# Optimization experiments

Hardware: AMD Instinct MI355X
Metric: run time of the kernel (lower is better)

Reference implementation:

```python
import jax, jax.numpy as jnp
import numpy as np

B, D, H, K = 2048, 1024, 64, 3
SKIP = 4  # first 4 dims only accumulate into ai, produce no heads


def setup_inputs() -> dict:
    key = jax.random.key(0)
    ks = jax.random.split(key, 6)
    return {
        "x": jax.random.normal(ks[0], (B, D), jnp.float32),
        "W": jax.random.normal(ks[1], (H, D), jnp.float32) * (2.0 / (H + 1)) ** 0.5,
        "c": jax.random.normal(ks[2], (1, H), jnp.float32) * 0.0,
        "Vmean": jax.random.normal(ks[3], (D, H, K), jnp.float32) * (2.0 / (H + K)) ** 0.5,
        "Valpha": jax.random.normal(ks[4], (D, H, K), jnp.float32) * (2.0 / (H + K)) ** 0.5,
        "Vstd": jax.random.normal(ks[5], (D, H, K), jnp.float32) * (2.0 / (H + K)) ** 0.5,
        "bmean": jnp.zeros((D, K), jnp.float32),
        "balpha": jnp.zeros((D, K), jnp.float32),
        "bstd": jnp.zeros((D, K), jnp.float32),
    }


def reference(x, W, c, Vmean, Valpha, Vstd, bmean, balpha, bstd):
    # ai before processing dim d is c + sum_{j<d} x[:, j] * W[:, j]^T.
    # This is a cumulative sum of per-dim rank-1 contributions -> one cumsum.
    contrib = x[:, :, None] * W.T[None, :, :]          # [B, D, H]
    prefix = c[None, :, :] + jnp.cumsum(contrib, axis=1)  # prefix[:, d] = c + sum_{j<=d}
    # h_i for dim d (d >= SKIP) uses ai = prefix[:, d-1]
    h = jax.nn.relu(prefix[:, SKIP - 1:-1, :])          # [B, D-SKIP, H]

    mean = jnp.einsum("bdh,dhk->bdk", h, Vmean[SKIP:]) + bmean[SKIP:]
    std = jax.nn.sigmoid(
        jnp.einsum("bdh,dhk->bdk", h, Vstd[SKIP:]) + bstd[SKIP:]
    ) * 2.0 + 0.6  # 10**-1 + 0.5
    alpha = jax.nn.softmax(
        jnp.einsum("bdh,dhk->bdk", h, Valpha[SKIP:]) + balpha[SKIP:], axis=-1
    )
    return (mean, std, alpha)  # each [B, D-4, K]
```

## Files before the change

### kernel.cpp

```cpp
#include <hip/hip_runtime.h>
#include <hip/hip_bf16.h>

#define B 2048
#define D 1024
#define H 64
#define DOUT (D - 4)
#define T 64
#define DC 16

typedef __attribute__((ext_vector_type(8))) short short8;
typedef __attribute__((ext_vector_type(4))) float f32x4;

#define WS_S  0
#define WS_VB (T * B * H / 2)

__device__ __forceinline__ unsigned short f2h_u(float f) {
    union { _Float16 h; unsigned short u; } v; v.h = (_Float16)f; return v.u;
}
__device__ __forceinline__ float h2f_u(unsigned short s) {
    union { unsigned short u; _Float16 h; } v; v.u = s; return (float)v.h;
}
__device__ __forceinline__ unsigned short f2bf(float f) {
    union { float f; unsigned int u; } v; v.f = f;
    unsigned int r = (v.u + 0x7FFFu + ((v.u >> 16) & 1u)) >> 16;
    return (unsigned short)r;
}
__device__ __forceinline__ unsigned cvtpk_bf16(float lo, float hi) {
    unsigned d;
    asm("v_cvt_pk_bf16_f32 %0, %1, %2" : "=v"(d) : "v"(lo), "v"(hi));
    return d;
}

union U8 { unsigned u[4]; short8 s; };

__global__ __launch_bounds__(256) void k_pack(const float* __restrict__ Vm,
                                              const float* __restrict__ Va,
                                              const float* __restrict__ Vs,
                                              uint4* __restrict__ VbP) {
    const int idx = blockIdx.x * 256 + threadIdx.x;
    const int l   = idx & 63;
    const int ks  = (idx >> 6) & 1;
    const int d   = idx >> 7;
    const int m   = l & 15;
    const int h0  = ks * 32 + (l >> 4) * 8;

    const float* src = nullptr;
    int k = 0;
    if (m < 3)                { src = Vm; k = m; }
    else if (m >= 4 && m < 7) { src = Vs; k = m - 4; }
    else if (m >= 8 && m < 11){ src = Va; k = m - 8; }

    unsigned u[4] = {0u, 0u, 0u, 0u};
    if (src) {
#pragma unroll
        for (int i = 0; i < 4; ++i) {
            unsigned short lo = f2bf(src[((size_t)d * H + h0 + 2 * i) * 3 + k]);
            unsigned short hi = f2bf(src[((size_t)d * H + h0 + 2 * i + 1) * 3 + k]);
            u[i] = ((unsigned)hi << 16) | lo;
        }
    }
    VbP[idx] = make_uint4(u[0], u[1], u[2], u[3]);
}

__global__ __launch_bounds__(512) void k_prefix(const float* __restrict__ x,
                                                const float* __restrict__ W,
                                                const float* __restrict__ cvec,
                                                unsigned short* __restrict__ S) {
    __shared__ float wt[64 * 68];
    __shared__ float xl[8 * 64];
    const int tid  = threadIdx.x;
    const int lane = tid & 63;
    const int w    = tid >> 6;
    const int b    = blockIdx.x * 8 + w;

    float run = cvec[lane];
    for (int c = 0; c < 16; ++c) {
        __syncthreads();
        {
            const int h = tid >> 3, dc = (tid & 7) * 8;
            const float* src = W + (size_t)h * D + c * 64 + dc;
            float4 v0 = *(const float4*)src;
            float4 v1 = *(const float4*)(src + 4);
            float* dst = wt + h * 68 + dc;
            *(float4*)dst = v0;
            *(float4*)(dst + 4) = v1;
        }
        xl[w * 64 + lane] = x[(size_t)b * D + c * 64 + lane];
        __syncthreads();
#pragma unroll
        for (int dg = 0; dg < 16; ++dg) {
            if ((dg & 3) == 1) {
                const int t = 4 * c + (dg >> 2);
                S[((size_t)t * B + b) * H + lane] = f2h_u(run);
            }
            float4 w4 = *(const float4*)(wt + lane * 68 + dg * 4);
            float4 x4 = *(const float4*)(xl + w * 64 + dg * 4);
            run = fmaf(x4.x, w4.x, run);
            run = fmaf(x4.y, w4.y, run);
            run = fmaf(x4.z, w4.z, run);
            run = fmaf(x4.w, w4.w, run);
        }
    }
}

__global__ __launch_bounds__(256, 2) void k_main(const float* __restrict__ x,
                                                 const float* __restrict__ W,
                                                 const unsigned short* __restrict__ S,
                                                 const uint4* __restrict__ VbP,
                                                 const float* __restrict__ bm,
                                                 const float* __restrict__ ba,
                                                 const float* __restrict__ bs,
                                                 float* __restrict__ out) {
    __shared__ short8 vbsh[DC][2][64];
    __shared__ float  wshf[DC][64];
    __shared__ float  xsf[DC][256];
    __shared__ float  bshf[DC][16];

    const int tid    = threadIdx.x;
    const int lane   = tid & 63;
    const int w      = tid >> 6;
    const int t      = blockIdx.y;
    const int bx     = blockIdx.x;
    const int dstart = 16 * t + 4;
    const int dvalid = D - dstart;
    const int r      = lane & 15;
    const int qq     = lane >> 4;

    {
        const uint4* vsrc = VbP + (size_t)dstart * 128;
        uint4* vdst = (uint4*)vbsh;
#pragma unroll
        for (int q = 0; q < 8; ++q) {
            const int j = q * 256 + tid;
            if (j < dvalid * 128) vdst[j] = vsrc[j];
        }
        {
            const int h = tid >> 2, part = tid & 3;
            if (dstart + part * 4 < D) {
                float4 v = *(const float4*)(W + (size_t)h * D + dstart + part * 4);
                wshf[part * 4 + 0][h] = v.x;
                wshf[part * 4 + 1][h] = v.y;
                wshf[part * 4 + 2][h] = v.z;
                wshf[part * 4 + 3][h] = v.w;
            }
        }
        {
            const float* xr = x + (size_t)(bx * 256 + tid) * D + dstart;
#pragma unroll
            for (int part = 0; part < 4; ++part) {
                if (dstart + part * 4 < D) {
                    float4 v = *(const float4*)(xr + part * 4);
                    xsf[part * 4 + 0][tid] = v.x;
                    xsf[part * 4 + 1][tid] = v.y;
                    xsf[part * 4 + 2][tid] = v.z;
                    xsf[part * 4 + 3][tid] = v.w;
                }
            }
        }
        {
            const int dl = tid >> 4, m = tid & 15;
            const int d = dstart + dl;
            float v = 0.f;
            if (d < D) {
                if (m < 3)                 v = bm[(size_t)d * 3 + m];
                else if (m >= 4 && m < 7)  v = bs[(size_t)d * 3 + m - 4];
                else if (m >= 8 && m < 11) v = ba[(size_t)d * 3 + m - 8];
            }
            bshf[dl][m] = v;
        }
    }

    float a_[4][2][8];
#pragma unroll
    for (int bt = 0; bt < 4; ++bt) {
#pragma unroll
        for (int ks = 0; ks < 2; ++ks) {
            const unsigned short* sp =
                S + ((size_t)t * B + bx * 256 + w * 64 + bt * 16 + r) * H + ks * 32 + qq * 8;
            uint4 u = *(const uint4*)sp;
            a_[bt][ks][0] = h2f_u((unsigned short)(u.x & 0xffff));
            a_[bt][ks][1] = h2f_u((unsigned short)(u.x >> 16));
            a_[bt][ks][2] = h2f_u((unsigned short)(u.y & 0xffff));
            a_[bt][ks][3] = h2f_u((unsigned short)(u.y >> 16));
            a_[bt][ks][4] = h2f_u((unsigned short)(u.z & 0xffff));
            a_[bt][ks][5] = h2f_u((unsigned short)(u.z >> 16));
            a_[bt][ks][6] = h2f_u((unsigned short)(u.w & 0xffff));
            a_[bt][ks][7] = h2f_u((unsigned short)(u.w >> 16));
        }
    }
    __syncthreads();

    const int nq = (t == T - 1) ? 3 : 4;
    for (int qd = 0; qd < nq; ++qd) {
        float buf[4][12];
#pragma unroll
        for (int d4 = 0; d4 < 4; ++d4) {
            const int dl = qd * 4 + d4;

            U8 bf[4][2];
#pragma unroll
            for (int bt = 0; bt < 4; ++bt)
#pragma unroll
                for (int ks = 0; ks < 2; ++ks)
#pragma unroll
                    for (int i = 0; i < 4; ++i)
                        bf[bt][ks].u[i] = cvtpk_bf16(fmaxf(a_[bt][ks][2 * i], 0.f),
                                                     fmaxf(a_[bt][ks][2 * i + 1], 0.f));

            short8 A0 = vbsh[dl][0][lane];
            short8 A1 = vbsh[dl][1][lane];
            f32x4 bias4 = ((const f32x4*)&bshf[dl][0])[qq];

            f32x4 acc[4];
#pragma unroll
            for (int bt = 0; bt < 4; ++bt) {
                acc[bt] = __builtin_amdgcn_mfma_f32_16x16x32_bf16(A0, bf[bt][0].s, bias4, 0, 0, 0);
                acc[bt] = __builtin_amdgcn_mfma_f32_16x16x32_bf16(A1, bf[bt][1].s, acc[bt], 0, 0, 0);
            }

#pragma unroll
            for (int bt = 0; bt < 4; ++bt) {
                float z0 = acc[bt][0], z1 = acc[bt][1], z2 = acc[bt][2];
                float o0 = z0, o1 = z1, o2 = z2;
                if (qq == 1) {
                    o0 = 2.f * __builtin_amdgcn_rcpf(1.f + __expf(-z0)) + 0.6f;
                    o1 = 2.f * __builtin_amdgcn_rcpf(1.f + __expf(-z1)) + 0.6f;
                    o2 = 2.f * __builtin_amdgcn_rcpf(1.f + __expf(-z2)) + 0.6f;
                } else if (qq == 2) {
                    float mx = fmaxf(z0, fmaxf(z1, z2));
                    float e0 = __expf(z0 - mx);
                    float e1 = __expf(z1 - mx);
                    float e2 = __expf(z2 - mx);
                    float inv = __builtin_amdgcn_rcpf(e0 + e1 + e2);
                    o0 = e0 * inv; o1 = e1 * inv; o2 = e2 * inv;
                }
                buf[bt][d4 * 3 + 0] = o0;
                buf[bt][d4 * 3 + 1] = o1;
                buf[bt][d4 * 3 + 2] = o2;
            }

            float4 w0a = *(const float4*)&wshf[dl][qq * 8];
            float4 w0b = *(const float4*)&wshf[dl][qq * 8 + 4];
            float4 w1a = *(const float4*)&wshf[dl][32 + qq * 8];
            float4 w1b = *(const float4*)&wshf[dl][32 + qq * 8 + 4];
#pragma unroll
            for (int bt = 0; bt < 4; ++bt) {
                const float xv = xsf[dl][w * 64 + bt * 16 + r];
                a_[bt][0][0] = fmaf(xv, w0a.x, a_[bt][0][0]);
                a_[bt][0][1] = fmaf(xv, w0a.y, a_[bt][0][1]);
                a_[bt][0][2] = fmaf(xv, w0a.z, a_[bt][0][2]);
                a_[bt][0][3] = fmaf(xv, w0a.w, a_[bt][0][3]);
                a_[bt][0][4] = fmaf(xv, w0b.x, a_[bt][0][4]);
                a_[bt][0][5] = fmaf(xv, w0b.y, a_[bt][0][5]);
                a_[bt][0][6] = fmaf(xv, w0b.z, a_[bt][0][6]);
                a_[bt][0][7] = fmaf(xv, w0b.w, a_[bt][0][7]);
                a_[bt][1][0] = fmaf(xv, w1a.x, a_[bt][1][0]);
                a_[bt][1][1] = fmaf(xv, w1a.y, a_[bt][1][1]);
                a_[bt][1][2] = fmaf(xv, w1a.z, a_[bt][1][2]);
                a_[bt][1][3] = fmaf(xv, w1a.w, a_[bt][1][3]);
                a_[bt][1][4] = fmaf(xv, w1b.x, a_[bt][1][4]);
                a_[bt][1][5] = fmaf(xv, w1b.y, a_[bt][1][5]);
                a_[bt][1][6] = fmaf(xv, w1b.z, a_[bt][1][6]);
                a_[bt][1][7] = fmaf(xv, w1b.w, a_[bt][1][7]);
            }
        }

        if (qq < 3) {
            float* ob = out + (size_t)qq * ((size_t)B * DOUT * 3);
            const size_t ioff = (size_t)(16 * t + 4 * qd) * 3;
#pragma unroll
            for (int bt = 0; bt < 4; ++bt) {
                float* p = ob + (size_t)(bx * 256 + w * 64 + bt * 16 + r) * (DOUT * 3) + ioff;
                *(float4*)(p + 0) = make_float4(buf[bt][0], buf[bt][1], buf[bt][2], buf[bt][3]);
                *(float4*)(p + 4) = make_float4(buf[bt][4], buf[bt][5], buf[bt][6], buf[bt][7]);
                *(float4*)(p + 8) = make_float4(buf[bt][8], buf[bt][9], buf[bt][10], buf[bt][11]);
            }
        }
    }
}

extern "C" void kernel_launch(void* const* d_in, const int* in_sizes, int n_in,
                              void* d_out, int out_size, void* d_ws, size_t ws_size,
                              hipStream_t stream) {
    const float* x  = (const float*)d_in[0];
    const float* W  = (const float*)d_in[1];
    const float* c  = (const float*)d_in[2];
    const float* Vm = (const float*)d_in[3];
    const float* Va = (const float*)d_in[4];
    const float* Vs = (const float*)d_in[5];
    const float* bm = (const float*)d_in[6];
    const float* ba = (const float*)d_in[7];
    const float* bs = (const float*)d_in[8];
    float* out = (float*)d_out;

    float* wsf = (float*)d_ws;
    unsigned short* S = (unsigned short*)(wsf + WS_S);
    uint4* VbP = (uint4*)(wsf + WS_VB);

    k_pack<<<dim3(D * 2 * 64 / 256), dim3(256), 0, stream>>>(Vm, Va, Vs, VbP);
    k_prefix<<<dim3(B / 8), dim3(512), 0, stream>>>(x, W, c, S);
    k_main<<<dim3(B / 256, T), dim3(256), 0, stream>>>(x, W, S, VbP, bm, ba, bs, out);
}
```

Measured before the change: 163.3 us.

## Halve dims per main block, precompute fp16 transposed W, simplify prefix scan

```diff
diff --git a/kernel.cpp b/kernel.cpp
--- a/kernel.cpp
+++ b/kernel.cpp
@@ -5,14 +5,15 @@
 #define D 1024
 #define H 64
 #define DOUT (D - 4)
-#define T 64
-#define DC 16
+#define T 128
+#define DC 8
 
 typedef __attribute__((ext_vector_type(8))) short short8;
 typedef __attribute__((ext_vector_type(4))) float f32x4;
 
 #define WS_S  0
 #define WS_VB (T * B * H / 2)
+#define WS_WT (WS_VB + D * 2 * 64 * 4)
 
 __device__ __forceinline__ unsigned short f2h_u(float f) {
     union { _Float16 h; unsigned short u; } v; v.h = (_Float16)f; return v.u;
@@ -33,78 +34,80 @@
 
 union U8 { unsigned u[4]; short8 s; };
 
-__global__ __launch_bounds__(256) void k_pack(const float* __restrict__ Vm,
+__global__ __launch_bounds__(256) void k_prep(const float* __restrict__ Vm,
                                               const float* __restrict__ Va,
                                               const float* __restrict__ Vs,
-                                              uint4* __restrict__ VbP) {
-    const int idx = blockIdx.x * 256 + threadIdx.x;
-    const int l   = idx & 63;
-    const int ks  = (idx >> 6) & 1;
-    const int d   = idx >> 7;
-    const int m   = l & 15;
-    const int h0  = ks * 32 + (l >> 4) * 8;
-
-    const float* src = nullptr;
-    int k = 0;
-    if (m < 3)                { src = Vm; k = m; }
-    else if (m >= 4 && m < 7) { src = Vs; k = m - 4; }
-    else if (m >= 8 && m < 11){ src = Va; k = m - 8; }
-
-    unsigned u[4] = {0u, 0u, 0u, 0u};
-    if (src) {
-#pragma unroll
-        for (int i = 0; i < 4; ++i) {
-            unsigned short lo = f2bf(src[((size_t)d * H + h0 + 2 * i) * 3 + k]);
-            unsigned short hi = f2bf(src[((size_t)d * H + h0 + 2 * i + 1) * 3 + k]);
-            u[i] = ((unsigned)hi << 16) | lo;
-        }
-    }
-    VbP[idx] = make_uint4(u[0], u[1], u[2], u[3]);
-}
-
-__global__ __launch_bounds__(512) void k_prefix(const float* __restrict__ x,
-                                                const float* __restrict__ W,
+                                              const float* __restrict__ W,
+                                              uint4* __restrict__ VbP,
+                                              unsigned short* __restrict__ Wth) {
+    __shared__ float tile[64][65];
+    const int tid = threadIdx.x;
+    const int bid = blockIdx.x;
+    if (bid < 512) {
+        const int idx = bid * 256 + tid;
+        const int l   = idx & 63;
+        const int ks  = (idx >> 6) & 1;
+        const int d   = idx >> 7;
+        const int m   = l & 15;
+        const int h0  = ks * 32 + (l >> 4) * 8;
+
+        const float* src = nullptr;
+        int k = 0;
+        if (m < 3)                 { src = Vm; k = m; }
+        else if (m >= 4 && m < 7)  { src = Vs; k = m - 4; }
+        else if (m >= 8 && m < 11) { src = Va; k = m - 8; }
+
+        unsigned u[4] = {0u, 0u, 0u, 0u};
+        if (src) {
+#pragma unroll
+            for (int i = 0; i < 4; ++i) {
+                unsigned short lo = f2bf(src[((size_t)d * H + h0 + 2 * i) * 3 + k]);
+                unsigned short hi = f2bf(src[((size_t)d * H + h0 + 2 * i + 1) * 3 + k]);
+                u[i] = ((unsigned)hi << 16) | lo;
+            }
+        }
+        VbP[idx] = make_uint4(u[0], u[1], u[2], u[3]);
+    } else {
+        const int d0 = (bid - 512) * 64;
+        const int tx = tid & 63;
+        const int ty = tid >> 6;
+#pragma unroll
+        for (int r = 0; r < 64; r += 4)
+            tile[r + ty][tx] = W[(size_t)(r + ty) * D + d0 + tx];
+        __syncthreads();
+#pragma unroll
+        for (int r = 0; r < 64; r += 4)
+            Wth[(size_t)(d0 + r + ty) * H + tx] = f2h_u(tile[tx][r + ty]);
+    }
+}
+
+__global__ __launch_bounds__(256) void k_prefix(const float* __restrict__ x,
+                                                const unsigned short* __restrict__ Wth,
                                                 const float* __restrict__ cvec,
                                                 unsigned short* __restrict__ S) {
-    __shared__ float wt[64 * 68];
-    __shared__ float xl[8 * 64];
-    const int tid  = threadIdx.x;
-    const int lane = tid & 63;
-    const int w    = tid >> 6;
-    const int b    = blockIdx.x * 8 + w;
+    const int lane = threadIdx.x & 63;
+    const int w    = threadIdx.x >> 6;
+    const int b    = blockIdx.x * 4 + w;
 
     float run = cvec[lane];
+    const float* xr = x + (size_t)b * D;
+    float xv = xr[lane];
     for (int c = 0; c < 16; ++c) {
-        __syncthreads();
-        {
-            const int h = tid >> 3, dc = (tid & 7) * 8;
-            const float* src = W + (size_t)h * D + c * 64 + dc;
-            float4 v0 = *(const float4*)src;
-            float4 v1 = *(const float4*)(src + 4);
-            float* dst = wt + h * 68 + dc;
-            *(float4*)dst = v0;
-            *(float4*)(dst + 4) = v1;
-        }
-        xl[w * 64 + lane] = x[(size_t)b * D + c * 64 + lane];
-        __syncthreads();
-#pragma unroll
-        for (int dg = 0; dg < 16; ++dg) {
-            if ((dg & 3) == 1) {
-                const int t = 4 * c + (dg >> 2);
-                S[((size_t)t * B + b) * H + lane] = f2h_u(run);
-            }
-            float4 w4 = *(const float4*)(wt + lane * 68 + dg * 4);
-            float4 x4 = *(const float4*)(xl + w * 64 + dg * 4);
-            run = fmaf(x4.x, w4.x, run);
-            run = fmaf(x4.y, w4.y, run);
-            run = fmaf(x4.z, w4.z, run);
-            run = fmaf(x4.w, w4.w, run);
-        }
-    }
-}
-
-__global__ __launch_bounds__(256, 2) void k_main(const float* __restrict__ x,
-                                                 const float* __restrict__ W,
+        const float xnext = (c < 15) ? xr[(c + 1) * 64 + lane] : 0.f;
+#pragma unroll
+        for (int j = 0; j < 64; ++j) {
+            const int d = c * 64 + j;
+            if ((d & 7) == 4)
+                S[((size_t)(d >> 3) * B + b) * H + lane] = f2h_u(run);
+            const float wv = h2f_u(Wth[(size_t)d * H + lane]);
+            run = fmaf(__shfl(xv, j), wv, run);
+        }
+        xv = xnext;
+    }
+}
+
+__global__ __launch_bounds__(256, 4) void k_main(const float* __restrict__ x,
+                                                 const unsigned short* __restrict__ Wth,
                                                  const unsigned short* __restrict__ S,
                                                  const uint4* __restrict__ VbP,
                                                  const float* __restrict__ bm,
@@ -121,7 +124,7 @@
     const int w      = tid >> 6;
     const int t      = blockIdx.y;
     const int bx     = blockIdx.x;
-    const int dstart = 16 * t + 4;
+    const int dstart = 8 * t + 4;
     const int dvalid = D - dstart;
     const int r      = lane & 15;
     const int qq     = lane >> 4;
@@ -130,26 +133,25 @@
         const uint4* vsrc = VbP + (size_t)dstart * 128;
         uint4* vdst = (uint4*)vbsh;
 #pragma unroll
-        for (int q = 0; q < 8; ++q) {
+        for (int q = 0; q < 4; ++q) {
             const int j = q * 256 + tid;
             if (j < dvalid * 128) vdst[j] = vsrc[j];
         }
         {
-            const int h = tid >> 2, part = tid & 3;
-            if (dstart + part * 4 < D) {
-                float4 v = *(const float4*)(W + (size_t)h * D + dstart + part * 4);
-                wshf[part * 4 + 0][h] = v.x;
-                wshf[part * 4 + 1][h] = v.y;
-                wshf[part * 4 + 2][h] = v.z;
-                wshf[part * 4 + 3][h] = v.w;
+            const unsigned* wsrc = (const unsigned*)(Wth + (size_t)dstart * H);
+            if (tid < dvalid * 32) {
+                const unsigned u = wsrc[tid];
+                const int dl = tid >> 5, h = (tid & 31) * 2;
+                wshf[dl][h]     = h2f_u((unsigned short)(u & 0xffff));
+                wshf[dl][h + 1] = h2f_u((unsigned short)(u >> 16));
             }
         }
         {
-            const float* xr = x + (size_t)(bx * 256 + tid) * D + dstart;
-#pragma unroll
-            for (int part = 0; part < 4; ++part) {
-                if (dstart + part * 4 < D) {
-                    float4 v = *(const float4*)(xr + part * 4);
+            const float* xr2 = x + (size_t)(bx * 256 + tid) * D + dstart;
+#pragma unroll
+            for (int part = 0; part < 2; ++part) {
+                if (part * 4 < dvalid) {
+                    float4 v = *(const float4*)(xr2 + part * 4);
                     xsf[part * 4 + 0][tid] = v.x;
                     xsf[part * 4 + 1][tid] = v.y;
                     xsf[part * 4 + 2][tid] = v.z;
@@ -158,15 +160,17 @@
             }
         }
         {
-            const int dl = tid >> 4, m = tid & 15;
-            const int d = dstart + dl;
-            float v = 0.f;
-            if (d < D) {
-                if (m < 3)                 v = bm[(size_t)d * 3 + m];
-                else if (m >= 4 && m < 7)  v = bs[(size_t)d * 3 + m - 4];
-                else if (m >= 8 && m < 11) v = ba[(size_t)d * 3 + m - 8];
-            }
-            bshf[dl][m] = v;
+            if (tid < DC * 16) {
+                const int dl = tid >> 4, m = tid & 15;
+                const int d = dstart + dl;
+                float v = 0.f;
+                if (d < D) {
+                    if (m < 3)                 v = bm[(size_t)d * 3 + m];
+                    else if (m >= 4 && m < 7)  v = bs[(size_t)d * 3 + m - 4];
+                    else if (m >= 8 && m < 11) v = ba[(size_t)d * 3 + m - 8];
+                }
+                bshf[dl][m] = v;
+            }
         }
     }
 
@@ -190,7 +194,7 @@
     }
     __syncthreads();
 
-    const int nq = (t == T - 1) ? 3 : 4;
+    const int nq = (t == T - 1) ? 1 : 2;
     for (int qd = 0; qd < nq; ++qd) {
         float buf[4][12];
 #pragma unroll
@@ -267,7 +271,7 @@
 
         if (qq < 3) {
             float* ob = out + (size_t)qq * ((size_t)B * DOUT * 3);
-            const size_t ioff = (size_t)(16 * t + 4 * qd) * 3;
+            const size_t ioff = (size_t)(8 * t + 4 * qd) * 3;
 #pragma unroll
             for (int bt = 0; bt < 4; ++bt) {
                 float* p = ob + (size_t)(bx * 256 + w * 64 + bt * 16 + r) * (DOUT * 3) + ioff;
@@ -296,8 +300,9 @@
     float* wsf = (float*)d_ws;
     unsigned short* S = (unsigned short*)(wsf + WS_S);
     uint4* VbP = (uint4*)(wsf + WS_VB);
-
-    k_pack<<<dim3(D * 2 * 64 / 256), dim3(256), 0, stream>>>(Vm, Va, Vs, VbP);
-    k_prefix<<<dim3(B / 8), dim3(512), 0, stream>>>(x, W, c, S);
-    k_main<<<dim3(B / 256, T), dim3(256), 0, stream>>>(x, W, S, VbP, bm, ba, bs, out);
-}
+    unsigned short* Wth = (unsigned short*)(wsf + WS_WT);
+
+    k_prep<<<dim3(512 + 16), dim3(256), 0, stream>>>(Vm, Va, Vs, W, VbP, Wth);
+    k_prefix<<<dim3(B / 4), dim3(256), 0, stream>>>(x, Wth, c, S);
+    k_main<<<dim3(B / 256, T), dim3(256), 0, stream>>>(x, Wth, S, VbP, bm, ba, bs, out);
+}
```

Result: slower. 233.4 us (+42.9%).
